# Kernel tuning notes

Hardware: AMD Instinct MI355X
Metric: run time of the kernel (lower is better)

## Reference

```python
import jax, jax.numpy as jnp
import numpy as np

EMBED_DIM = 1024


def _lru_init(d, seed=0):
    rng = np.random.default_rng(seed)
    r_min, r_max = 0.9, 0.999
    u1 = rng.random(d)
    u2 = rng.random(d)
    nu_log = np.log(-0.5 * np.log(u1 * (r_max ** 2 - r_min ** 2) + r_min ** 2))
    theta_log = np.log(u2 * np.pi * 2)
    gamma_log = np.log(np.sqrt(1 - np.exp(-np.exp(nu_log)) ** 2))
    return theta_log.astype(np.float32), gamma_log.astype(np.float32)


def setup_inputs() -> dict:
    key = jax.random.key(0)
    ks = jax.random.split(key, 8)
    d = EMBED_DIM
    b, n = 4, 4096
    theta_log, gamma_log = _lru_init(d)
    s = 1.0 / np.sqrt(d)
    s2 = 1.0 / np.sqrt(2 * d)
    return {
        "x": jax.random.normal(ks[0], (b, n, d), dtype=jnp.float32),
        "theta_log": jnp.asarray(theta_log),
        "gamma_log": jnp.asarray(gamma_log),
        "nu_w": jax.random.uniform(ks[1], (d, d), minval=-s, maxval=s, dtype=jnp.float32),
        "nu_b": jax.random.uniform(ks[2], (d,), minval=-s, maxval=s, dtype=jnp.float32),
        "in_w": jax.random.uniform(ks[3], (2 * d, d), minval=-s, maxval=s, dtype=jnp.float32),
        "in_b": jax.random.uniform(ks[4], (2 * d,), minval=-s, maxval=s, dtype=jnp.float32),
        "out_w": jax.random.uniform(ks[5], (d, 2 * d), minval=-s2, maxval=s2, dtype=jnp.float32),
        "out_b": jax.random.uniform(ks[6], (d,), minval=-s2, maxval=s2, dtype=jnp.float32),
    }


def reference(x, theta_log, gamma_log, nu_w, nu_b, in_w, in_b, out_w, out_b):
    # x: (b, n, d) -> (n, b, d)
    xt = jnp.transpose(x, (1, 0, 2))
    n, b, d = xt.shape
    input_state = jnp.einsum("nbd,ed->nbe", xt, in_w) + in_b  # (n, b, 2d)
    nu = jax.nn.sigmoid(jnp.einsum("nbd,ed->nbe", xt, nu_w) + nu_b)  # (n, b, d)
    theta = jnp.exp(theta_log)  # (d,)
    gamma = jnp.exp(gamma_log)  # (d,)
    lam_r = nu * jnp.cos(theta)  # (n, b, d)
    lam_i = nu * jnp.sin(theta)
    # 'n b (e k) -> n b e k' with k=2: even idx = real, odd = imag
    ist = input_state.reshape(n, b, d, 2)
    u_r = gamma * ist[..., 0]
    u_i = gamma * ist[..., 1]

    def step(carry, inp):
        hr, hi = carry
        lr, li, ur, ui = inp
        nhr = lr * hr - li * hi + ur
        nhi = lr * hi + li * hr + ui
        return (nhr, nhi), (nhr, nhi)

    h0 = (jnp.zeros((b, d), x.dtype), jnp.zeros((b, d), x.dtype))
    _, (h_r, h_i) = jax.lax.scan(step, h0, (lam_r, lam_i, u_r, u_i))
    feature = jnp.concatenate([h_r, h_i], axis=-1)  # (n, b, 2d)
    out = jnp.einsum("nbe,de->nbd", feature, out_w) + out_b
    return jnp.transpose(out, (1, 0, 2))  # (b, n, d)
```

## Files before the change

### kernel.cpp

```cpp
#include <hip/hip_runtime.h>
#include <math.h>
#include <stdint.h>

#define BB 4
#define NN 4096
#define DD 1024
#define TT (BB * NN)
#define NC 64
#define CL (NN / NC)

typedef __attribute__((ext_vector_type(8))) short bf16x8;
typedef __attribute__((ext_vector_type(4))) float f32x4;

__device__ inline unsigned short bf_rne(float v) {
  union { float f; uint32_t u; } x; x.f = v;
  uint32_t r = x.u + 0x7fffu + ((x.u >> 16) & 1u);
  return (unsigned short)(r >> 16);
}
__device__ inline float bf_to_f(unsigned short h) {
  union { float f; uint32_t u; } x; x.u = ((uint32_t)h) << 16;
  return x.f;
}

__device__ inline void async16(const void* g, void* l) {
  __builtin_amdgcn_global_load_lds(
      (const __attribute__((address_space(1))) uint32_t*)g,
      (__attribute__((address_space(3))) uint32_t*)l, 16, 0, 0);
}

__global__ __launch_bounds__(256) void conv_x_kernel(
    const float* __restrict__ x, unsigned short* __restrict__ Abf) {
  int idx = blockIdx.x * 256 + threadIdx.x;
  int k = idx & 1023;
  int n = (idx >> 10) & 4095;
  int b = idx >> 22;
  Abf[(size_t)(n * 4 + b) * 1024 + k] = bf_rne(x[idx]);
}

__global__ __launch_bounds__(256) void conv_w1_kernel(
    const float* __restrict__ in_w, const float* __restrict__ nu_w,
    unsigned short* __restrict__ W1) {
  int idx = blockIdx.x * 256 + threadIdx.x;
  float v = (idx < 2048 * 1024) ? in_w[idx] : nu_w[idx - 2048 * 1024];
  W1[idx] = bf_rne(v);
}

__global__ __launch_bounds__(256) void conv_w2_kernel(
    const float* __restrict__ out_w, unsigned short* __restrict__ W2) {
  int idx = blockIdx.x * 256 + threadIdx.x;
  int j = idx >> 10, d = idx & 1023;
  W2[(size_t)j * 2048 + 2 * d]     = bf_rne(out_w[(size_t)j * 2048 + d]);
  W2[(size_t)j * 2048 + 2 * d + 1] = bf_rne(out_w[(size_t)j * 2048 + 1024 + d]);
}

__global__ __launch_bounds__(512, 2) void gemm1_mfma(
    const unsigned short* __restrict__ A,
    const unsigned short* __restrict__ W1,
    const float* __restrict__ in_b, const float* __restrict__ nu_b,
    const float* __restrict__ gamma_log,
    unsigned short* __restrict__ U16, _Float16* __restrict__ NU) {
  __shared__ unsigned short As[2][16384];
  __shared__ unsigned short Bs[2][16384];
  const int tid = threadIdx.x;
  const int w = tid >> 6, l = tid & 63;
  const int q = l >> 4, ml = l & 15;
  const int m0 = blockIdx.y * 256;
  const int n0 = blockIdx.x * 256;
  const int wm = w & 1, wn = w >> 1;

  f32x4 acc[8][4] = {};

  auto stage = [&](int p, int k0) {
#pragma unroll
    for (int rg = 0; rg < 4; ++rg) {
      async16(A  + (size_t)(m0 + rg * 64 + l) * 1024 + k0 + w * 8,
              &As[p][(w * 256 + rg * 64) * 8]);
      async16(W1 + (size_t)(n0 + rg * 64 + l) * 1024 + k0 + w * 8,
              &Bs[p][(w * 256 + rg * 64) * 8]);
    }
  };

  stage(0, 0);
  int cur = 0;
  for (int k0 = 0; k0 < 1024; k0 += 64) {
    if (k0 + 64 < 1024) {
      stage(cur ^ 1, k0 + 64);
      asm volatile("s_waitcnt vmcnt(8)" ::: "memory");
    } else {
      asm volatile("s_waitcnt vmcnt(0)" ::: "memory");
    }
    __builtin_amdgcn_s_barrier();
    __builtin_amdgcn_sched_barrier(0);
#pragma unroll
    for (int ks = 0; ks < 2; ++ks) {
      bf16x8 af[8], bfr[4];
#pragma unroll
      for (int i = 0; i < 8; ++i)
        af[i] = *(const bf16x8*)&As[cur][(((ks * 4 + q) * 256) + wm * 128 + i * 16 + ml) * 8];
#pragma unroll
      for (int j = 0; j < 4; ++j)
        bfr[j] = *(const bf16x8*)&Bs[cur][(((ks * 4 + q) * 256) + wn * 64 + j * 16 + ml) * 8];
#pragma unroll
      for (int i = 0; i < 8; ++i)
#pragma unroll
        for (int j = 0; j < 4; ++j)
          acc[i][j] = __builtin_amdgcn_mfma_f32_16x16x32_bf16(af[i], bfr[j], acc[i][j], 0, 0, 0);
    }
    __builtin_amdgcn_sched_barrier(0);
    __builtin_amdgcn_s_barrier();
    cur ^= 1;
  }

  if (n0 < 2048) {
#pragma unroll
    for (int j = 0; j < 4; ++j) {
      int col = n0 + wn * 64 + j * 16 + ml;
      float bias = in_b[col];
      float gam = expf(gamma_log[col >> 1]);
#pragma unroll
      for (int i = 0; i < 8; ++i) {
        int trow = m0 + wm * 128 + i * 16 + q * 4;
#pragma unroll
        for (int v = 0; v < 4; ++v)
          U16[(size_t)(trow + v) * 2048 + col] = bf_rne(gam * (acc[i][j][v] + bias));
      }
    }
  } else {
#pragma unroll
    for (int j = 0; j < 4; ++j) {
      int col = n0 + wn * 64 + j * 16 + ml;
      int c2 = col - 2048;
      float bias = nu_b[c2];
#pragma unroll
      for (int i = 0; i < 8; ++i) {
        int trow = m0 + wm * 128 + i * 16 + q * 4;
#pragma unroll
        for (int v = 0; v < 4; ++v) {
          float z = acc[i][j][v] + bias;
          NU[(size_t)(trow + v) * 1024 + c2] = (_Float16)(1.f / (1.f + expf(-z)));
        }
      }
    }
  }
}

__global__ __launch_bounds__(256) void scan_p1_kernel(
    const unsigned short* __restrict__ U16, const _Float16* __restrict__ NU,
    const float* __restrict__ theta_log,
    float* __restrict__ chunkA) {
  int s = blockIdx.x * 256 + threadIdx.x;
  int dch = s & (DD - 1);
  int b = (s >> 10) & (BB - 1);
  int c = s >> 12;
  float theta = expf(theta_log[dch]);
  float ct = cosf(theta), st = sinf(theta);
  float hr = 0.f, hi = 0.f, Ar = 1.f, Ai = 0.f;
  for (int i = 0; i < CL; ++i) {
    int t = (c * CL + i) * 4 + b;
    ushort2 up = *(const ushort2*)(U16 + (size_t)t * 2048 + 2 * dch);
    float ur = bf_to_f(up.x), ui = bf_to_f(up.y);
    float nu = (float)NU[(size_t)t * 1024 + dch];
    float lr = nu * ct, li = nu * st;
    float hr2 = lr * hr - li * hi + ur;
    float hi2 = lr * hi + li * hr + ui;
    hr = hr2; hi = hi2;
    float Ar2 = lr * Ar - li * Ai;
    float Ai2 = lr * Ai + li * Ar;
    Ar = Ar2; Ai = Ai2;
  }
  float4 o = {Ar, Ai, hr, hi};
  *(float4*)(chunkA + (size_t)s * 4) = o;
}

__global__ __launch_bounds__(256) void scan_p2_kernel(
    float* __restrict__ chunkA) {
  int qx = blockIdx.x * 256 + threadIdx.x;
  int dch = qx & (DD - 1);
  int b = qx >> 10;
  float cr = 0.f, ci = 0.f;
  for (int c = 0; c < NC; ++c) {
    size_t idx = ((size_t)(c * BB + b) * DD + dch) * 4;
    float4 v = *(const float4*)(chunkA + idx);
    float2 wv = {cr, ci};
    *(float2*)(chunkA + idx + 2) = wv;
    float nr = v.x * cr - v.y * ci + v.z;
    float ni = v.x * ci + v.y * cr + v.w;
    cr = nr; ci = ni;
  }
}

__global__ __launch_bounds__(256) void scan_p3_kernel(
    unsigned short* __restrict__ U16, const _Float16* __restrict__ NU,
    const float* __restrict__ theta_log, const float* __restrict__ chunkA) {
  const int c = blockIdx.x >> 2, b = blockIdx.x & 3;
  const int tid = threadIdx.x;
  float ct[4], st[4], hr[4], hi_[4];
#pragma unroll
  for (int dj = 0; dj < 4; ++dj) {
    int d = tid * 4 + dj;
    float th = expf(theta_log[d]);
    ct[dj] = cosf(th); st[dj] = sinf(th);
    const float* cp = chunkA + ((size_t)((c * 4 + b) * 1024) + d) * 4 + 2;
    hr[dj] = cp[0]; hi_[dj] = cp[1];
  }
  for (int i = 0; i < CL; ++i) {
    int t = (c * CL + i) * 4 + b;
    unsigned short* up = U16 + (size_t)t * 2048 + 8 * tid;
    bf16x8 uv = *(const bf16x8*)up;
    const _Float16* nup = NU + (size_t)t * 1024 + 4 * tid;
    bf16x8 fo;
#pragma unroll
    for (int dj = 0; dj < 4; ++dj) {
      float nu = (float)nup[dj];
      float lr = nu * ct[dj], li = nu * st[dj];
      float nhr = lr * hr[dj] - li * hi_[dj] + bf_to_f((unsigned short)uv[2 * dj]);
      float nhi = lr * hi_[dj] + li * hr[dj] + bf_to_f((unsigned short)uv[2 * dj + 1]);
      hr[dj] = nhr; hi_[dj] = nhi;
      fo[2 * dj] = (short)bf_rne(nhr);
      fo[2 * dj + 1] = (short)bf_rne(nhi);
    }
    *(bf16x8*)up = fo;
  }
}

__global__ __launch_bounds__(512, 2) void gemm2_mfma(
    const unsigned short* __restrict__ F,
    const unsigned short* __restrict__ W2,
    const float* __restrict__ out_b,
    float* __restrict__ out) {
  __shared__ unsigned short As[2][16384];
  __shared__ unsigned short Bs[2][16384];
  const int tid = threadIdx.x;
  const int w = tid >> 6, l = tid & 63;
  const int q = l >> 4, ml = l & 15;
  const int m0 = blockIdx.y * 256;
  const int n0 = blockIdx.x * 256;
  const int wm = w & 1, wn = w >> 1;

  f32x4 acc[8][4] = {};

  auto stage = [&](int p, int k0) {
#pragma unroll
    for (int rg = 0; rg < 4; ++rg) {
      async16(F  + (size_t)(m0 + rg * 64 + l) * 2048 + k0 + w * 8,
              &As[p][(w * 256 + rg * 64) * 8]);
      async16(W2 + (size_t)(n0 + rg * 64 + l) * 2048 + k0 + w * 8,
              &Bs[p][(w * 256 + rg * 64) * 8]);
    }
  };

  stage(0, 0);
  int cur = 0;
  for (int k0 = 0; k0 < 2048; k0 += 64) {
    if (k0 + 64 < 2048) {
      stage(cur ^ 1, k0 + 64);
      asm volatile("s_waitcnt vmcnt(8)" ::: "memory");
    } else {
      asm volatile("s_waitcnt vmcnt(0)" ::: "memory");
    }
    __builtin_amdgcn_s_barrier();
    __builtin_amdgcn_sched_barrier(0);
#pragma unroll
    for (int ks = 0; ks < 2; ++ks) {
      bf16x8 af[8], bfr[4];
#pragma unroll
      for (int i = 0; i < 8; ++i)
        af[i] = *(const bf16x8*)&As[cur][(((ks * 4 + q) * 256) + wm * 128 + i * 16 + ml) * 8];
#pragma unroll
      for (int j = 0; j < 4; ++j)
        bfr[j] = *(const bf16x8*)&Bs[cur][(((ks * 4 + q) * 256) + wn * 64 + j * 16 + ml) * 8];
#pragma unroll
      for (int i = 0; i < 8; ++i)
#pragma unroll
        for (int j = 0; j < 4; ++j)
          acc[i][j] = __builtin_amdgcn_mfma_f32_16x16x32_bf16(af[i], bfr[j], acc[i][j], 0, 0, 0);
    }
    __builtin_amdgcn_sched_barrier(0);
    __builtin_amdgcn_s_barrier();
    cur ^= 1;
  }

#pragma unroll
  for (int j = 0; j < 4; ++j) {
    int col = n0 + wn * 64 + j * 16 + ml;
    float bias = out_b[col];
#pragma unroll
    for (int i = 0; i < 8; ++i) {
      int trow = m0 + wm * 128 + i * 16 + q * 4;
#pragma unroll
      for (int v = 0; v < 4; ++v) {
        int t = trow + v;
        out[((size_t)(t & 3) * NN + (t >> 2)) * DD + col] = acc[i][j][v] + bias;
      }
    }
  }
}

extern "C" void kernel_launch(void* const* d_in, const int* in_sizes, int n_in,
                              void* d_out, int out_size, void* d_ws, size_t ws_size,
                              hipStream_t stream) {
  const float* x         = (const float*)d_in[0];
  const float* theta_log = (const float*)d_in[1];
  const float* gamma_log = (const float*)d_in[2];
  const float* nu_w      = (const float*)d_in[3];
  const float* nu_b      = (const float*)d_in[4];
  const float* in_w      = (const float*)d_in[5];
  const float* in_b      = (const float*)d_in[6];
  const float* out_w     = (const float*)d_in[7];
  const float* out_b     = (const float*)d_in[8];
  float* out = (float*)d_out;

  char* base = (char*)d_ws;
  unsigned short* U16 = (unsigned short*)base;
  _Float16*       NU  = (_Float16*)(base + 67108864);
  unsigned short* Abf = (unsigned short*)(base + 100663296);
  unsigned short* W1  = (unsigned short*)(base + 134217728);
  unsigned short* W2  = (unsigned short*)(base + 140509184);
  float*          chunkA = (float*)(base + 144703488);

  conv_x_kernel<<<(BB * NN * DD) / 256, 256, 0, stream>>>(x, Abf);
  conv_w1_kernel<<<(3072 * 1024) / 256, 256, 0, stream>>>(in_w, nu_w, W1);
  conv_w2_kernel<<<(1024 * 1024) / 256, 256, 0, stream>>>(out_w, W2);
  gemm1_mfma<<<dim3(3072 / 256, TT / 256), 512, 0, stream>>>(
      Abf, W1, in_b, nu_b, gamma_log, U16, NU);
  scan_p1_kernel<<<(NC * BB * DD) / 256, 256, 0, stream>>>(U16, NU, theta_log, chunkA);
  scan_p2_kernel<<<(BB * DD) / 256, 256, 0, stream>>>(chunkA);
  scan_p3_kernel<<<NC * BB, 256, 0, stream>>>(U16, NU, theta_log, chunkA);
  gemm2_mfma<<<dim3(1024 / 256, TT / 256), 512, 0, stream>>>(U16, W2, out_b, out);
}
```

Baseline: 511.9 us.

## Halve GEMM K-tile, raise occupancy, and remap blocks for XCD locality

After: 1.311 ms. +156.1%, slower.

```diff
diff --git a/kernel.cpp b/kernel.cpp
--- a/kernel.cpp
+++ b/kernel.cpp
@@ -53,53 +53,58 @@
   W2[(size_t)j * 2048 + 2 * d + 1] = bf_rne(out_w[(size_t)j * 2048 + 1024 + d]);
 }
 
-__global__ __launch_bounds__(512, 2) void gemm1_mfma(
+__global__ __launch_bounds__(512, 4) void gemm1_mfma(
     const unsigned short* __restrict__ A,
     const unsigned short* __restrict__ W1,
     const float* __restrict__ in_b, const float* __restrict__ nu_b,
     const float* __restrict__ gamma_log,
     unsigned short* __restrict__ U16, _Float16* __restrict__ NU) {
-  __shared__ unsigned short As[2][16384];
-  __shared__ unsigned short Bs[2][16384];
+  __shared__ unsigned short As[2][8192];
+  __shared__ unsigned short Bs[2][8192];
   const int tid = threadIdx.x;
   const int w = tid >> 6, l = tid & 63;
   const int q = l >> 4, ml = l & 15;
-  const int m0 = blockIdx.y * 256;
-  const int n0 = blockIdx.x * 256;
+  const int orig = blockIdx.x + gridDim.x * blockIdx.y;
+  const int xcd = orig & 7;
+  const int jj_ = orig >> 3;
+  const int ntile = jj_ >> 3;
+  const int mloc = jj_ & 7;
+  const int m0 = (xcd * 8 + mloc) * 256;
+  const int n0 = ntile * 256;
   const int wm = w & 1, wn = w >> 1;
 
   f32x4 acc[8][4] = {};
 
   auto stage = [&](int p, int k0) {
-#pragma unroll
-    for (int rg = 0; rg < 4; ++rg) {
-      async16(A  + (size_t)(m0 + rg * 64 + l) * 1024 + k0 + w * 8,
-              &As[p][(w * 256 + rg * 64) * 8]);
-      async16(W1 + (size_t)(n0 + rg * 64 + l) * 1024 + k0 + w * 8,
-              &Bs[p][(w * 256 + rg * 64) * 8]);
-    }
+    const int kq = w & 3;
+    const unsigned short* src = (w < 4) ? A : W1;
+    unsigned short* dst = (w < 4) ? &As[p][0] : &Bs[p][0];
+    const int base = (w < 4) ? m0 : n0;
+#pragma unroll
+    for (int rg = 0; rg < 4; ++rg)
+      async16(src + (size_t)(base + rg * 64 + l) * 1024 + k0 + kq * 8,
+              dst + (kq * 256 + rg * 64) * 8);
   };
 
   stage(0, 0);
   int cur = 0;
-  for (int k0 = 0; k0 < 1024; k0 += 64) {
-    if (k0 + 64 < 1024) {
-      stage(cur ^ 1, k0 + 64);
-      asm volatile("s_waitcnt vmcnt(8)" ::: "memory");
+  for (int k0 = 0; k0 < 1024; k0 += 32) {
+    if (k0 + 32 < 1024) {
+      stage(cur ^ 1, k0 + 32);
+      asm volatile("s_waitcnt vmcnt(4)" ::: "memory");
     } else {
       asm volatile("s_waitcnt vmcnt(0)" ::: "memory");
     }
     __builtin_amdgcn_s_barrier();
     __builtin_amdgcn_sched_barrier(0);
-#pragma unroll
-    for (int ks = 0; ks < 2; ++ks) {
+    {
       bf16x8 af[8], bfr[4];
 #pragma unroll
       for (int i = 0; i < 8; ++i)
-        af[i] = *(const bf16x8*)&As[cur][(((ks * 4 + q) * 256) + wm * 128 + i * 16 + ml) * 8];
+        af[i] = *(const bf16x8*)&As[cur][((q * 256) + wm * 128 + i * 16 + ml) * 8];
 #pragma unroll
       for (int j = 0; j < 4; ++j)
-        bfr[j] = *(const bf16x8*)&Bs[cur][(((ks * 4 + q) * 256) + wn * 64 + j * 16 + ml) * 8];
+        bfr[j] = *(const bf16x8*)&Bs[cur][((q * 256) + wn * 64 + j * 16 + ml) * 8];
 #pragma unroll
       for (int i = 0; i < 8; ++i)
 #pragma unroll
@@ -223,52 +228,57 @@
   }
 }
 
-__global__ __launch_bounds__(512, 2) void gemm2_mfma(
+__global__ __launch_bounds__(512, 4) void gemm2_mfma(
     const unsigned short* __restrict__ F,
     const unsigned short* __restrict__ W2,
     const float* __restrict__ out_b,
     float* __restrict__ out) {
-  __shared__ unsigned short As[2][16384];
-  __shared__ unsigned short Bs[2][16384];
+  __shared__ unsigned short As[2][8192];
+  __shared__ unsigned short Bs[2][8192];
   const int tid = threadIdx.x;
   const int w = tid >> 6, l = tid & 63;
   const int q = l >> 4, ml = l & 15;
-  const int m0 = blockIdx.y * 256;
-  const int n0 = blockIdx.x * 256;
+  const int orig = blockIdx.x + gridDim.x * blockIdx.y;
+  const int xcd = orig & 7;
+  const int jj_ = orig >> 3;
+  const int mloc = jj_ >> 2;
+  const int ntile = jj_ & 3;
+  const int m0 = (xcd * 8 + mloc) * 256;
+  const int n0 = ntile * 256;
   const int wm = w & 1, wn = w >> 1;
 
   f32x4 acc[8][4] = {};
 
   auto stage = [&](int p, int k0) {
-#pragma unroll
-    for (int rg = 0; rg < 4; ++rg) {
-      async16(F  + (size_t)(m0 + rg * 64 + l) * 2048 + k0 + w * 8,
-              &As[p][(w * 256 + rg * 64) * 8]);
-      async16(W2 + (size_t)(n0 + rg * 64 + l) * 2048 + k0 + w * 8,
-              &Bs[p][(w * 256 + rg * 64) * 8]);
-    }
+    const int kq = w & 3;
+    const unsigned short* src = (w < 4) ? F : W2;
+    unsigned short* dst = (w < 4) ? &As[p][0] : &Bs[p][0];
+    const int base = (w < 4) ? m0 : n0;
+#pragma unroll
+    for (int rg = 0; rg < 4; ++rg)
+      async16(src + (size_t)(base + rg * 64 + l) * 2048 + k0 + kq * 8,
+              dst + (kq * 256 + rg * 64) * 8);
   };
 
   stage(0, 0);
   int cur = 0;
-  for (int k0 = 0; k0 < 2048; k0 += 64) {
-    if (k0 + 64 < 2048) {
-      stage(cur ^ 1, k0 + 64);
-      asm volatile("s_waitcnt vmcnt(8)" ::: "memory");
+  for (int k0 = 0; k0 < 2048; k0 += 32) {
+    if (k0 + 32 < 2048) {
+      stage(cur ^ 1, k0 + 32);
+      asm volatile("s_waitcnt vmcnt(4)" ::: "memory");
     } else {
       asm volatile("s_waitcnt vmcnt(0)" ::: "memory");
     }
     __builtin_amdgcn_s_barrier();
     __builtin_amdgcn_sched_barrier(0);
-#pragma unroll
-    for (int ks = 0; ks < 2; ++ks) {
+    {
       bf16x8 af[8], bfr[4];
 #pragma unroll
       for (int i = 0; i < 8; ++i)
-        af[i] = *(const bf16x8*)&As[cur][(((ks * 4 + q) * 256) + wm * 128 + i * 16 + ml) * 8];
+        af[i] = *(const bf16x8*)&As[cur][((q * 256) + wm * 128 + i * 16 + ml) * 8];
 #pragma unroll
       for (int j = 0; j < 4; ++j)
-        bfr[j] = *(const bf16x8*)&Bs[cur][(((ks * 4 + q) * 256) + wn * 64 + j * 16 + ml) * 8];
+        bfr[j] = *(const bf16x8*)&Bs[cur][((q * 256) + wn * 64 + j * 16 + ml) * 8];
 #pragma unroll
       for (int i = 0; i < 8; ++i)
 #pragma unroll
```

## Interleave prefetch with MFMA phases and remap blocks per XCD in both GEMMs

Applied to the files above, without the earlier changes.

New measurement: 490.9 us. -4.1%, faster.

```diff
diff --git a/kernel.cpp b/kernel.cpp
--- a/kernel.cpp
+++ b/kernel.cpp
@@ -64,50 +64,68 @@
   const int tid = threadIdx.x;
   const int w = tid >> 6, l = tid & 63;
   const int q = l >> 4, ml = l & 15;
-  const int m0 = blockIdx.y * 256;
-  const int n0 = blockIdx.x * 256;
+  const int orig = blockIdx.x + gridDim.x * blockIdx.y;
+  const int xcd = orig & 7;
+  const int jj_ = orig >> 3;
+  const int ntile = jj_ >> 3;
+  const int mloc = jj_ & 7;
+  const int m0 = (xcd * 8 + mloc) * 256;
+  const int n0 = ntile * 256;
   const int wm = w & 1, wn = w >> 1;
 
   f32x4 acc[8][4] = {};
 
-  auto stage = [&](int p, int k0) {
-#pragma unroll
-    for (int rg = 0; rg < 4; ++rg) {
-      async16(A  + (size_t)(m0 + rg * 64 + l) * 1024 + k0 + w * 8,
-              &As[p][(w * 256 + rg * 64) * 8]);
-      async16(W1 + (size_t)(n0 + rg * 64 + l) * 1024 + k0 + w * 8,
-              &Bs[p][(w * 256 + rg * 64) * 8]);
-    }
+  auto stage_part = [&](int p, int k0, int c) {
+    async16(A  + (size_t)(m0 + c * 64 + l) * 1024 + k0 + w * 8,
+            &As[p][(w * 256 + c * 64) * 8]);
+    async16(W1 + (size_t)(n0 + c * 64 + l) * 1024 + k0 + w * 8,
+            &Bs[p][(w * 256 + c * 64) * 8]);
   };
 
-  stage(0, 0);
+#pragma unroll
+  for (int c = 0; c < 4; ++c) stage_part(0, 0, c);
+
   int cur = 0;
   for (int k0 = 0; k0 < 1024; k0 += 64) {
-    if (k0 + 64 < 1024) {
-      stage(cur ^ 1, k0 + 64);
-      asm volatile("s_waitcnt vmcnt(8)" ::: "memory");
+    const bool last = (k0 + 64 >= 1024);
+    if (!last) {
+      stage_part(cur ^ 1, k0 + 64, 0);
+      asm volatile("s_waitcnt vmcnt(2)" ::: "memory");
     } else {
       asm volatile("s_waitcnt vmcnt(0)" ::: "memory");
     }
     __builtin_amdgcn_s_barrier();
     __builtin_amdgcn_sched_barrier(0);
+
+    bf16x8 bfr[4], af[4];
 #pragma unroll
     for (int ks = 0; ks < 2; ++ks) {
-      bf16x8 af[8], bfr[4];
-#pragma unroll
-      for (int i = 0; i < 8; ++i)
-        af[i] = *(const bf16x8*)&As[cur][(((ks * 4 + q) * 256) + wm * 128 + i * 16 + ml) * 8];
-#pragma unroll
-      for (int j = 0; j < 4; ++j)
-        bfr[j] = *(const bf16x8*)&Bs[cur][(((ks * 4 + q) * 256) + wn * 64 + j * 16 + ml) * 8];
-#pragma unroll
-      for (int i = 0; i < 8; ++i)
-#pragma unroll
-        for (int j = 0; j < 4; ++j)
-          acc[i][j] = __builtin_amdgcn_mfma_f32_16x16x32_bf16(af[i], bfr[j], acc[i][j], 0, 0, 0);
-    }
-    __builtin_amdgcn_sched_barrier(0);
-    __builtin_amdgcn_s_barrier();
+#pragma unroll
+      for (int mh = 0; mh < 2; ++mh) {
+        if (mh == 0) {
+#pragma unroll
+          for (int j = 0; j < 4; ++j)
+            bfr[j] = *(const bf16x8*)&Bs[cur][(((ks * 4 + q) * 256) + wn * 64 + j * 16 + ml) * 8];
+        }
+#pragma unroll
+        for (int i = 0; i < 4; ++i)
+          af[i] = *(const bf16x8*)&As[cur][(((ks * 4 + q) * 256) + wm * 128 + mh * 64 + i * 16 + ml) * 8];
+        const int ph = ks * 2 + mh;
+        if (!last && ph < 3) stage_part(cur ^ 1, k0 + 64, ph + 1);
+        asm volatile("s_waitcnt lgkmcnt(0)" ::: "memory");
+        __builtin_amdgcn_sched_barrier(0);
+        __builtin_amdgcn_s_setprio(1);
+#pragma unroll
+        for (int i = 0; i < 4; ++i)
+#pragma unroll
+          for (int j = 0; j < 4; ++j)
+            acc[mh * 4 + i][j] = __builtin_amdgcn_mfma_f32_16x16x32_bf16(
+                af[i], bfr[j], acc[mh * 4 + i][j], 0, 0, 0);
+        __builtin_amdgcn_s_setprio(0);
+        __builtin_amdgcn_sched_barrier(0);
+        __builtin_amdgcn_s_barrier();
+      }
+    }
     cur ^= 1;
   }
 
@@ -233,50 +251,68 @@
   const int tid = threadIdx.x;
   const int w = tid >> 6, l = tid & 63;
   const int q = l >> 4, ml = l & 15;
-  const int m0 = blockIdx.y * 256;
-  const int n0 = blockIdx.x * 256;
+  const int orig = blockIdx.x + gridDim.x * blockIdx.y;
+  const int xcd = orig & 7;
+  const int jj_ = orig >> 3;
+  const int mloc = jj_ >> 2;
+  const int ntile = jj_ & 3;
+  const int m0 = (xcd * 8 + mloc) * 256;
+  const int n0 = ntile * 256;
   const int wm = w & 1, wn = w >> 1;
 
   f32x4 acc[8][4] = {};
 
-  auto stage = [&](int p, int k0) {
-#pragma unroll
-    for (int rg = 0; rg < 4; ++rg) {
-      async16(F  + (size_t)(m0 + rg * 64 + l) * 2048 + k0 + w * 8,
-              &As[p][(w * 256 + rg * 64) * 8]);
-      async16(W2 + (size_t)(n0 + rg * 64 + l) * 2048 + k0 + w * 8,
-              &Bs[p][(w * 256 + rg * 64) * 8]);
-    }
+  auto stage_part = [&](int p, int k0, int c) {
+    async16(F  + (size_t)(m0 + c * 64 + l) * 2048 + k0 + w * 8,
+            &As[p][(w * 256 + c * 64) * 8]);
+    async16(W2 + (size_t)(n0 + c * 64 + l) * 2048 + k0 + w * 8,
+            &Bs[p][(w * 256 + c * 64) * 8]);
   };
 
-  stage(0, 0);
+#pragma unroll
+  for (int c = 0; c < 4; ++c) stage_part(0, 0, c);
+
   int cur = 0;
   for (int k0 = 0; k0 < 2048; k0 += 64) {
-    if (k0 + 64 < 2048) {
-      stage(cur ^ 1, k0 + 64);
-      asm volatile("s_waitcnt vmcnt(8)" ::: "memory");
+    const bool last = (k0 + 64 >= 2048);
+    if (!last) {
+      stage_part(cur ^ 1, k0 + 64, 0);
+      asm volatile("s_waitcnt vmcnt(2)" ::: "memory");
     } else {
       asm volatile("s_waitcnt vmcnt(0)" ::: "memory");
     }
     __builtin_amdgcn_s_barrier();
     __builtin_amdgcn_sched_barrier(0);
+
+    bf16x8 bfr[4], af[4];
 #pragma unroll
     for (int ks = 0; ks < 2; ++ks) {
-      bf16x8 af[8], bfr[4];
-#pragma unroll
-      for (int i = 0; i < 8; ++i)
-        af[i] = *(const bf16x8*)&As[cur][(((ks * 4 + q) * 256) + wm * 128 + i * 16 + ml) * 8];
-#pragma unroll
-      for (int j = 0; j < 4; ++j)
-        bfr[j] = *(const bf16x8*)&Bs[cur][(((ks * 4 + q) * 256) + wn * 64 + j * 16 + ml) * 8];
-#pragma unroll
-      for (int i = 0; i < 8; ++i)
-#pragma unroll
-        for (int j = 0; j < 4; ++j)
-          acc[i][j] = __builtin_amdgcn_mfma_f32_16x16x32_bf16(af[i], bfr[j], acc[i][j], 0, 0, 0);
-    }
-    __builtin_amdgcn_sched_barrier(0);
-    __builtin_amdgcn_s_barrier();
+#pragma unroll
+      for (int mh = 0; mh < 2; ++mh) {
+        if (mh == 0) {
+#pragma unroll
+          for (int j = 0; j < 4; ++j)
+            bfr[j] = *(const bf16x8*)&Bs[cur][(((ks * 4 + q) * 256) + wn * 64 + j * 16 + ml) * 8];
+        }
+#pragma unroll
+        for (int i = 0; i < 4; ++i)
+          af[i] = *(const bf16x8*)&As[cur][(((ks * 4 + q) * 256) + wm * 128 + mh * 64 + i * 16 + ml) * 8];
+        const int ph = ks * 2 + mh;
+        if (!last && ph < 3) stage_part(cur ^ 1, k0 + 64, ph + 1);
+        asm volatile("s_waitcnt lgkmcnt(0)" ::: "memory");
+        __builtin_amdgcn_sched_barrier(0);
+        __builtin_amdgcn_s_setprio(1);
+#pragma unroll
+        for (int i = 0; i < 4; ++i)
+#pragma unroll
+          for (int j = 0; j < 4; ++j)
+            acc[mh * 4 + i][j] = __builtin_amdgcn_mfma_f32_16x16x32_bf16(
+                af[i], bfr[j], acc[mh * 4 + i][j], 0, 0, 0);
+        __builtin_amdgcn_s_setprio(0);
+        __builtin_amdgcn_sched_barrier(0);
+        __builtin_amdgcn_s_barrier();
+      }
+    }
     cur ^= 1;
   }
 
```

## Load weight fragments directly from global and remap blocks per XCD

Applied to the files above, without the earlier changes.

Result: slower. 580.7 us (+13.5%).

```diff
diff --git a/kernel.cpp b/kernel.cpp
--- a/kernel.cpp
+++ b/kernel.cpp
@@ -60,32 +60,42 @@
     const float* __restrict__ gamma_log,
     unsigned short* __restrict__ U16, _Float16* __restrict__ NU) {
   __shared__ unsigned short As[2][16384];
-  __shared__ unsigned short Bs[2][16384];
   const int tid = threadIdx.x;
   const int w = tid >> 6, l = tid & 63;
   const int q = l >> 4, ml = l & 15;
-  const int m0 = blockIdx.y * 256;
-  const int n0 = blockIdx.x * 256;
+  const int orig = blockIdx.x + gridDim.x * blockIdx.y;
+  const int xcd = orig & 7;
+  const int jj_ = orig >> 3;
+  const int ntile = jj_ >> 3;
+  const int mloc = jj_ & 7;
+  const int m0 = (xcd * 8 + mloc) * 256;
+  const int n0 = ntile * 256;
   const int wm = w & 1, wn = w >> 1;
 
   f32x4 acc[8][4] = {};
 
-  auto stage = [&](int p, int k0) {
-#pragma unroll
-    for (int rg = 0; rg < 4; ++rg) {
-      async16(A  + (size_t)(m0 + rg * 64 + l) * 1024 + k0 + w * 8,
+  auto stageA = [&](int p, int k0) {
+#pragma unroll
+    for (int rg = 0; rg < 4; ++rg)
+      async16(A + (size_t)(m0 + rg * 64 + l) * 1024 + k0 + w * 8,
               &As[p][(w * 256 + rg * 64) * 8]);
-      async16(W1 + (size_t)(n0 + rg * 64 + l) * 1024 + k0 + w * 8,
-              &Bs[p][(w * 256 + rg * 64) * 8]);
-    }
   };
 
-  stage(0, 0);
+  const unsigned short* Bp = W1 + (size_t)(n0 + wn * 64 + ml) * 1024 + q * 8;
+
+  stageA(0, 0);
   int cur = 0;
   for (int k0 = 0; k0 < 1024; k0 += 64) {
-    if (k0 + 64 < 1024) {
-      stage(cur ^ 1, k0 + 64);
-      asm volatile("s_waitcnt vmcnt(8)" ::: "memory");
+    const bool last = (k0 + 64 >= 1024);
+    bf16x8 bfr[2][4];
+#pragma unroll
+    for (int ks = 0; ks < 2; ++ks)
+#pragma unroll
+      for (int j = 0; j < 4; ++j)
+        bfr[ks][j] = *(const bf16x8*)(Bp + (size_t)j * 16 * 1024 + k0 + ks * 32);
+    if (!last) {
+      stageA(cur ^ 1, k0 + 64);
+      asm volatile("s_waitcnt vmcnt(4)" ::: "memory");
     } else {
       asm volatile("s_waitcnt vmcnt(0)" ::: "memory");
     }
@@ -93,18 +103,15 @@
     __builtin_amdgcn_sched_barrier(0);
 #pragma unroll
     for (int ks = 0; ks < 2; ++ks) {
-      bf16x8 af[8], bfr[4];
+      bf16x8 af[8];
 #pragma unroll
       for (int i = 0; i < 8; ++i)
         af[i] = *(const bf16x8*)&As[cur][(((ks * 4 + q) * 256) + wm * 128 + i * 16 + ml) * 8];
 #pragma unroll
-      for (int j = 0; j < 4; ++j)
-        bfr[j] = *(const bf16x8*)&Bs[cur][(((ks * 4 + q) * 256) + wn * 64 + j * 16 + ml) * 8];
-#pragma unroll
       for (int i = 0; i < 8; ++i)
 #pragma unroll
         for (int j = 0; j < 4; ++j)
-          acc[i][j] = __builtin_amdgcn_mfma_f32_16x16x32_bf16(af[i], bfr[j], acc[i][j], 0, 0, 0);
+          acc[i][j] = __builtin_amdgcn_mfma_f32_16x16x32_bf16(af[i], bfr[ks][j], acc[i][j], 0, 0, 0);
     }
     __builtin_amdgcn_sched_barrier(0);
     __builtin_amdgcn_s_barrier();
@@ -229,32 +236,42 @@
     const float* __restrict__ out_b,
     float* __restrict__ out) {
   __shared__ unsigned short As[2][16384];
-  __shared__ unsigned short Bs[2][16384];
   const int tid = threadIdx.x;
   const int w = tid >> 6, l = tid & 63;
   const int q = l >> 4, ml = l & 15;
-  const int m0 = blockIdx.y * 256;
-  const int n0 = blockIdx.x * 256;
+  const int orig = blockIdx.x + gridDim.x * blockIdx.y;
+  const int xcd = orig & 7;
+  const int jj_ = orig >> 3;
+  const int mloc = jj_ >> 2;
+  const int ntile = jj_ & 3;
+  const int m0 = (xcd * 8 + mloc) * 256;
+  const int n0 = ntile * 256;
   const int wm = w & 1, wn = w >> 1;
 
   f32x4 acc[8][4] = {};
 
-  auto stage = [&](int p, int k0) {
-#pragma unroll
-    for (int rg = 0; rg < 4; ++rg) {
-      async16(F  + (size_t)(m0 + rg * 64 + l) * 2048 + k0 + w * 8,
+  auto stageA = [&](int p, int k0) {
+#pragma unroll
+    for (int rg = 0; rg < 4; ++rg)
+      async16(F + (size_t)(m0 + rg * 64 + l) * 2048 + k0 + w * 8,
               &As[p][(w * 256 + rg * 64) * 8]);
-      async16(W2 + (size_t)(n0 + rg * 64 + l) * 2048 + k0 + w * 8,
-              &Bs[p][(w * 256 + rg * 64) * 8]);
-    }
   };
 
-  stage(0, 0);
+  const unsigned short* Bp = W2 + (size_t)(n0 + wn * 64 + ml) * 2048 + q * 8;
+
+  stageA(0, 0);
   int cur = 0;
   for (int k0 = 0; k0 < 2048; k0 += 64) {
-    if (k0 + 64 < 2048) {
-      stage(cur ^ 1, k0 + 64);
-      asm volatile("s_waitcnt vmcnt(8)" ::: "memory");
+    const bool last = (k0 + 64 >= 2048);
+    bf16x8 bfr[2][4];
+#pragma unroll
+    for (int ks = 0; ks < 2; ++ks)
+#pragma unroll
+      for (int j = 0; j < 4; ++j)
+        bfr[ks][j] = *(const bf16x8*)(Bp + (size_t)j * 16 * 2048 + k0 + ks * 32);
+    if (!last) {
+      stageA(cur ^ 1, k0 + 64);
+      asm volatile("s_waitcnt vmcnt(4)" ::: "memory");
     } else {
       asm volatile("s_waitcnt vmcnt(0)" ::: "memory");
     }
@@ -262,18 +279,15 @@
     __builtin_amdgcn_sched_barrier(0);
 #pragma unroll
     for (int ks = 0; ks < 2; ++ks) {
-      bf16x8 af[8], bfr[4];
+      bf16x8 af[8];
 #pragma unroll
       for (int i = 0; i < 8; ++i)
         af[i] = *(const bf16x8*)&As[cur][(((ks * 4 + q) * 256) + wm * 128 + i * 16 + ml) * 8];
 #pragma unroll
-      for (int j = 0; j < 4; ++j)
-        bfr[j] = *(const bf16x8*)&Bs[cur][(((ks * 4 + q) * 256) + wn * 64 + j * 16 + ml) * 8];
-#pragma unroll
       for (int i = 0; i < 8; ++i)
 #pragma unroll
         for (int j = 0; j < 4; ++j)
-          acc[i][j] = __builtin_amdgcn_mfma_f32_16x16x32_bf16(af[i], bfr[j], acc[i][j], 0, 0, 0);
+          acc[i][j] = __builtin_amdgcn_mfma_f32_16x16x32_bf16(af[i], bfr[ks][j], acc[i][j], 0, 0, 0);
     }
     __builtin_amdgcn_sched_barrier(0);
     __builtin_amdgcn_s_barrier();
```
